# Kernel optimization log

Measured on AMD Instinct MI355X. Metric: run time of the kernel, lower is better.

Reference implementation:

```python
import jax, jax.numpy as jnp
import numpy as np

N = 100000      # nodes
E = 1_600_000   # edges (avg degree 16)
IN, HID, OUT = 128, 128, 64


def _prep(edge_index, n):
    """Add self-loops and compute symmetric GCN normalization per edge."""
    loops = jnp.arange(n, dtype=edge_index.dtype)
    src = jnp.concatenate([edge_index[0], loops])  # [E+N]
    dst = jnp.concatenate([edge_index[1], loops])  # [E+N]
    deg = jax.ops.segment_sum(jnp.ones(src.shape, jnp.float32), dst, num_segments=n)
    dinv = jnp.where(deg > 0, jax.lax.rsqrt(deg), 0.0)
    norm = dinv[src] * dinv[dst]                   # [E+N]
    return src, dst, norm


def gcn_conv(x, src, dst, norm, W, b, n):
    # PyG GCNConv: transform first, then normalized gather/scatter-add aggregate
    h = x @ W                                      # [N, C_out]
    msg = h[src] * norm[:, None]                   # [E+N, C_out] irregular gather
    return jax.ops.segment_sum(msg, dst, num_segments=n) + b


def setup_inputs() -> dict:
    key = jax.random.key(0)
    k1, k2, k3, k4 = jax.random.split(key, 4)
    x = jax.random.normal(k1, (N, IN), dtype=jnp.float32)
    edge_index = jax.random.randint(k2, (2, E), 0, N, dtype=jnp.int32)
    W1 = jax.random.normal(k3, (IN, HID), dtype=jnp.float32) * (1.0 / np.sqrt(IN))
    b1 = jnp.zeros((HID,), jnp.float32)
    W2 = jax.random.normal(k4, (HID, OUT), dtype=jnp.float32) * (1.0 / np.sqrt(HID))
    b2 = jnp.zeros((OUT,), jnp.float32)
    return {"x": x, "W1": W1, "b1": b1, "W2": W2, "b2": b2, "edge_index": edge_index}


def reference(x, W1, b1, W2, b2, edge_index):
    n = x.shape[0]
    src, dst, norm = _prep(edge_index, n)
    h = gcn_conv(x, src, dst, norm, W1, b1, n)
    h = jax.nn.softmax(h, axis=1)
    return gcn_conv(h, src, dst, norm, W2, b2, n)
```

## Files before the change

kernel.cpp:

```cpp
#include <hip/hip_runtime.h>
#include <hip/hip_fp16.h>
#include <cstdint>
#include <cstddef>


#define BSHIFT 8
#define NBPAD 512
#define NWG 256
#define CAP 6144

typedef _Float16 half8 __attribute__((ext_vector_type(8)));
typedef float f32x4 __attribute__((ext_vector_type(4)));

__device__ __forceinline__ void h8_to_f(const uint4& u, float* f) {
  const __half2* hp = (const __half2*)&u;
#pragma unroll
  for (int i = 0; i < 4; ++i) {
    float2 t = __half22float2(hp[i]);
    f[2 * i] = t.x;
    f[2 * i + 1] = t.y;
  }
}

__device__ __forceinline__ void fma8(float* acc, float w, const float* v) {
#pragma unroll
  for (int i = 0; i < 8; ++i) acc[i] = fmaf(w, v[i], acc[i]);
}

__device__ __forceinline__ int block_scan256(int v, int* wsums) {
  const int lane = threadIdx.x & 63;
  const int wid = threadIdx.x >> 6;
  int x = v;
#pragma unroll
  for (int d = 1; d < 64; d <<= 1) {
    int y = __shfl_up(x, d);
    if (lane >= d) x += y;
  }
  if (lane == 63) wsums[wid] = x;
  __syncthreads();
  int off = 0;
#pragma unroll
  for (int j = 0; j < 4; ++j)
    if (j < wid) off += wsums[j];
  return off + x;
}

__global__ __launch_bounds__(256) void wg_count(const int* __restrict__ dst,
                                                int* __restrict__ counts,
                                                int E, int nb, int slice) {
  __shared__ int lh[NBPAD];
  const int w = blockIdx.x;
  for (int i = threadIdx.x; i < nb; i += 256) lh[i] = 0;
  __syncthreads();
  const int e0 = w * slice;
  const int e1 = min(e0 + slice, E);
  for (int e = e0 + threadIdx.x; e < e1; e += 256)
    atomicAdd(&lh[dst[e] >> BSHIFT], 1);
  __syncthreads();
  for (int i = threadIdx.x; i < nb; i += 256) counts[(size_t)w * NBPAD + i] = lh[i];
}

__global__ __launch_bounds__(1024) void scan_buckets(const int* __restrict__ counts,
                                                     int* __restrict__ bstart,
                                                     int* __restrict__ row_start,
                                                     int nb, int n, int E) {
  __shared__ int wsum[16];
  const int tid = threadIdx.x;
  const int lane = tid & 63;
  const int wid = tid >> 6;
  int v = 0;
  if (tid < nb) {
#pragma unroll 4
    for (int i = 0; i < NWG; ++i) v += counts[(size_t)i * NBPAD + tid];
  }
  int x = v;
#pragma unroll
  for (int d = 1; d < 64; d <<= 1) {
    int y = __shfl_up(x, d);
    if (lane >= d) x += y;
  }
  if (lane == 63) wsum[wid] = x;
  __syncthreads();
  if (wid == 0) {
    int w = (lane < 16) ? wsum[lane] : 0;
#pragma unroll
    for (int d = 1; d < 16; d <<= 1) {
      int y = __shfl_up(w, d);
      if (lane >= d) w += y;
    }
    if (lane < 16) wsum[lane] = w;
  }
  __syncthreads();
  int boff = (wid > 0) ? wsum[wid - 1] : 0;
  int incl = boff + x;
  if (tid < nb) {
    bstart[tid] = incl - v;
    if (tid == nb - 1) bstart[nb] = incl;
  }
  if (tid == 0) row_start[n] = E;
}

__global__ __launch_bounds__(256) void cell_scan(const int* __restrict__ counts,
                                                 const int* __restrict__ bstart,
                                                 int* __restrict__ cur, int nb) {
  __shared__ int wsums[4];
  const int b = blockIdx.x;
  const int tid = threadIdx.x;
  int v = counts[(size_t)tid * NBPAD + b];
  int incl = block_scan256(v, wsums);
  cur[(size_t)tid * NBPAD + b] = bstart[b] + incl - v;
}

__global__ __launch_bounds__(256) void wg_scatter(const int* __restrict__ src,
                                                  const int* __restrict__ dst,
                                                  const int* __restrict__ cur,
                                                  unsigned* __restrict__ staging,
                                                  int E, int nb, int slice) {
  __shared__ int lc[NBPAD];
  const int w = blockIdx.x;
  for (int i = threadIdx.x; i < nb; i += 256) lc[i] = cur[(size_t)w * NBPAD + i];
  __syncthreads();
  const int e0 = w * slice;
  const int e1 = min(e0 + slice, E);
  for (int e = e0 + threadIdx.x; e < e1; e += 256) {
    int d = dst[e];
    int p = atomicAdd(&lc[d >> BSHIFT], 1);
    staging[p] = ((unsigned)(d & 255) << 24) | (unsigned)src[e];
  }
}

__global__ __launch_bounds__(256) void bucket_hist(const unsigned* __restrict__ staging,
                                                   const int* __restrict__ bstart,
                                                   int* __restrict__ row_start,
                                                   float* __restrict__ dinv, int n) {
  __shared__ int lcnt[256];
  __shared__ int wsums[4];
  const int b = blockIdx.x;
  const int tid = threadIdx.x;
  const int n0 = b << BSHIFT;
  const int s0 = bstart[b];
  const int cnt = bstart[b + 1] - s0;

  lcnt[tid] = 0;
  __syncthreads();
  for (int i = tid; i < cnt; i += 256)
    atomicAdd(&lcnt[staging[s0 + i] >> 24], 1);
  __syncthreads();

  const int v = lcnt[tid];
  const int incl = block_scan256(v, wsums);
  const int node = n0 + tid;
  if (node < n) {
    row_start[node] = s0 + incl - v;
    dinv[node] = rsqrtf((float)v + 1.0f);
  }
}

__global__ __launch_bounds__(256) void bucket_pack(const unsigned* __restrict__ staging,
                                                   const int* __restrict__ bstart,
                                                   const int* __restrict__ row_start,
                                                   const float* __restrict__ dinv,
                                                   int2* __restrict__ pack, int n) {
  __shared__ int lcur[256];
  __shared__ int lbuf[CAP];
  const int b = blockIdx.x;
  const int tid = threadIdx.x;
  const int n0 = b << BSHIFT;
  const int s0 = bstart[b];
  const int cnt = bstart[b + 1] - s0;

  const int node = n0 + tid;
  lcur[tid] = (node < n) ? (row_start[node] - s0) : 0;
  __syncthreads();

  for (int i = tid; i < cnt; i += 256) {
    unsigned p = staging[s0 + i];
    int pos = atomicAdd(&lcur[p >> 24], 1);
    int s = (int)(p & 0xFFFFFFu);
    if (pos < CAP) lbuf[pos] = s;
    else pack[s0 + pos] = make_int2(s, __float_as_int(dinv[s]));
  }
  __syncthreads();
  const int lim = cnt < CAP ? cnt : CAP;
  for (int i = tid; i < lim; i += 256) {
    int s = lbuf[i];
    pack[s0 + i] = make_int2(s, __float_as_int(dinv[s]));
  }
}

template <int M>
__global__ __launch_bounds__(256) void pack_w(const float* __restrict__ W,
                                              _Float16* __restrict__ Wp) {
  int e = blockIdx.x * 256 + threadIdx.x;
  if (e < 128 * M) {
    int k = e / M, c = e % M;
    int t = k >> 5, g = (k >> 3) & 3, j = k & 7;
    Wp[(((size_t)t * M + c) * 4 + g) * 8 + j] = (_Float16)W[e];
  }
}

template <int M, bool HIN>
__global__ __launch_bounds__(256) void gemm_mfma(const void* __restrict__ Xp,
                                                 const _Float16* __restrict__ Wp,
                                                 _Float16* __restrict__ H, int N) {
  constexpr int CT = M / 16;
  const int wave = threadIdx.x >> 6;
  const int lane = threadIdx.x & 63;
  const int row0 = (blockIdx.x * 4 + wave) * 16;
  if (row0 >= N) return;
  const int r = lane & 15;
  const int g = lane >> 4;
  int row = row0 + r;
  if (row >= N) row = N - 1;

  f32x4 acc[CT];
#pragma unroll
  for (int c = 0; c < CT; ++c) acc[c] = (f32x4){0.f, 0.f, 0.f, 0.f};

#pragma unroll
  for (int t = 0; t < 4; ++t) {
    half8 a;
    if constexpr (HIN) {
      a = *(const half8*)((const _Float16*)Xp + (size_t)row * 128 + t * 32 + g * 8);
    } else {
      const float* xp = (const float*)Xp + (size_t)row * 128 + t * 32 + g * 8;
      float4 x0 = *(const float4*)xp;
      float4 x1 = *(const float4*)(xp + 4);
      a[0] = (_Float16)x0.x; a[1] = (_Float16)x0.y;
      a[2] = (_Float16)x0.z; a[3] = (_Float16)x0.w;
      a[4] = (_Float16)x1.x; a[5] = (_Float16)x1.y;
      a[6] = (_Float16)x1.z; a[7] = (_Float16)x1.w;
    }
#pragma unroll
    for (int c = 0; c < CT; ++c) {
      half8 b = *(const half8*)(Wp + (((size_t)t * M + c * 16 + r) * 4 + g) * 8);
      acc[c] = __builtin_amdgcn_mfma_f32_16x16x32_f16(a, b, acc[c], 0, 0, 0);
    }
  }

#pragma unroll
  for (int c = 0; c < CT; ++c) {
#pragma unroll
    for (int i = 0; i < 4; ++i) {
      int rr = row0 + 4 * g + i;
      if (rr < N) H[(size_t)rr * M + c * 16 + r] = (_Float16)acc[c][i];
    }
  }
}

__device__ __forceinline__ void pack_batch(const int2* __restrict__ pack,
                                           int e, int e1, int2* p) {
#pragma unroll
  for (int j = 0; j < 4; ++j) {
    int idx = e + j;
    bool ok = idx < e1;
    p[j] = pack[ok ? idx : (e1 - 1)];
    if (!ok) p[j].y = 0;
  }
}

template <int F, bool SM, bool OUTHALF>
__global__ __launch_bounds__(256) void aggregate(const __half* __restrict__ h,
                                                 const int* __restrict__ row_start,
                                                 const int2* __restrict__ pack,
                                                 const float* __restrict__ dinv,
                                                 const float* __restrict__ bias,
                                                 void* __restrict__ out, int n) {
  constexpr int LPG = F / 8;
  constexpr int GPB = 256 / LPG;
  const int node = blockIdx.x * GPB + (int)(threadIdx.x / LPG);
  const int lane = threadIdx.x % LPG;
  if (node >= n) return;

  const uint4* hv = (const uint4*)h;
  const float di = dinv[node];

  float acc[8];
  {
    uint4 su = hv[(size_t)node * LPG + lane];
    float sf[8];
    h8_to_f(su, sf);
#pragma unroll
    for (int i = 0; i < 8; ++i) acc[i] = di * sf[i];
  }

  const int e0 = row_start[node];
  const int e1 = row_start[node + 1];
  if (e0 < e1) {
    int2 p[4];
    pack_batch(pack, e0, e1, p);
    int e = e0;
    for (;;) {
      uint4 r[4];
#pragma unroll
      for (int j = 0; j < 4; ++j) r[j] = hv[(size_t)p[j].x * LPG + lane];
      const int en = e + 4;
      const bool more = en < e1;
      int2 pn[4];
      if (more) pack_batch(pack, en, e1, pn);
#pragma unroll
      for (int j = 0; j < 4; ++j) {
        float v[8];
        h8_to_f(r[j], v);
        fma8(acc, __int_as_float(p[j].y), v);
      }
      if (!more) break;
#pragma unroll
      for (int j = 0; j < 4; ++j) p[j] = pn[j];
      e = en;
    }
  }

  {
    const float4* bv = (const float4*)bias;
    float4 b0 = bv[lane * 2], b1 = bv[lane * 2 + 1];
    acc[0] = fmaf(di, acc[0], b0.x);
    acc[1] = fmaf(di, acc[1], b0.y);
    acc[2] = fmaf(di, acc[2], b0.z);
    acc[3] = fmaf(di, acc[3], b0.w);
    acc[4] = fmaf(di, acc[4], b1.x);
    acc[5] = fmaf(di, acc[5], b1.y);
    acc[6] = fmaf(di, acc[6], b1.z);
    acc[7] = fmaf(di, acc[7], b1.w);
  }

  if constexpr (SM) {
    float m = acc[0];
#pragma unroll
    for (int i = 1; i < 8; ++i) m = fmaxf(m, acc[i]);
#pragma unroll
    for (int off = LPG / 2; off >= 1; off >>= 1) m = fmaxf(m, __shfl_xor(m, off));
    float ex[8], ssum = 0.f;
#pragma unroll
    for (int i = 0; i < 8; ++i) {
      ex[i] = __expf(acc[i] - m);
      ssum += ex[i];
    }
#pragma unroll
    for (int off = LPG / 2; off >= 1; off >>= 1) ssum += __shfl_xor(ssum, off);
    float r = 1.0f / ssum;
#pragma unroll
    for (int i = 0; i < 8; ++i) acc[i] = ex[i] * r;
  }

  if constexpr (OUTHALF) {
    union { __half2 h2[4]; uint4 u; } cv;
#pragma unroll
    for (int i = 0; i < 4; ++i)
      cv.h2[i] = __floats2half2_rn(acc[2 * i], acc[2 * i + 1]);
    ((uint4*)out)[(size_t)node * LPG + lane] = cv.u;
  } else {
    float4* ov = (float4*)out;
    ov[(size_t)node * (F / 4) + lane * 2] =
        make_float4(acc[0], acc[1], acc[2], acc[3]);
    ov[(size_t)node * (F / 4) + lane * 2 + 1] =
        make_float4(acc[4], acc[5], acc[6], acc[7]);
  }
}

extern "C" void kernel_launch(void* const* d_in, const int* in_sizes, int n_in,
                              void* d_out, int out_size, void* d_ws, size_t ws_size,
                              hipStream_t stream) {
  const float* x  = (const float*)d_in[0];
  const float* W1 = (const float*)d_in[1];
  const float* b1 = (const float*)d_in[2];
  const float* W2 = (const float*)d_in[3];
  const float* b2 = (const float*)d_in[4];
  const int*   ei = (const int*)d_in[5];

  const int N = in_sizes[0] / 128;
  const int E = in_sizes[5] / 2;
  const int NB = (N + 255) >> BSHIFT;
  const int SLICE = (E + NWG - 1) / NWG;
  const int* srcp = ei;
  const int* dstp = ei + E;

  auto align256 = [](size_t v) { return (v + 255) & ~(size_t)255; };
  char* ws = (char*)d_ws;
  size_t o_dinv   = 0;
  size_t o_rs     = align256(o_dinv + (size_t)N * 4);
  size_t o_cnts   = align256(o_rs + (size_t)(N + 1) * 4);
  size_t o_cur    = align256(o_cnts + (size_t)NWG * NBPAD * 4);
  size_t o_bstart = align256(o_cur + (size_t)NWG * NBPAD * 4);
  size_t o_wp1    = align256(o_bstart + (size_t)(NBPAD + 1) * 4);
  size_t o_wp2    = align256(o_wp1 + (size_t)128 * 128 * 2);
  size_t o_stg    = align256(o_wp2 + (size_t)128 * 64 * 2);
  size_t o_pack   = align256(o_stg + (size_t)E * 4);
  size_t o_h1     = align256(o_pack + (size_t)E * 8);
  size_t o_s      = align256(o_h1 + (size_t)N * 128 * 2);

  float*    dinv     = (float*)(ws + o_dinv);
  int*      rowstart = (int*)(ws + o_rs);
  int*      counts   = (int*)(ws + o_cnts);
  int*      cur      = (int*)(ws + o_cur);
  int*      bstart   = (int*)(ws + o_bstart);
  _Float16* wp1      = (_Float16*)(ws + o_wp1);
  _Float16* wp2      = (_Float16*)(ws + o_wp2);
  unsigned* staging  = (unsigned*)(ws + o_stg);
  int2*     pack     = (int2*)(ws + o_pack);
  _Float16* h1       = (_Float16*)(ws + o_h1);
  _Float16* sbuf     = (_Float16*)(ws + o_s);

  wg_count<<<NWG, 256, 0, stream>>>(dstp, counts, E, NB, SLICE);
  scan_buckets<<<1, 1024, 0, stream>>>(counts, bstart, rowstart, NB, N, E);
  cell_scan<<<NB, 256, 0, stream>>>(counts, bstart, cur, NB);
  wg_scatter<<<NWG, 256, 0, stream>>>(srcp, dstp, cur, staging, E, NB, SLICE);
  bucket_hist<<<NB, 256, 0, stream>>>(staging, bstart, rowstart, dinv, N);
  bucket_pack<<<NB, 256, 0, stream>>>(staging, bstart, rowstart, dinv, pack, N);

  pack_w<128><<<(128 * 128 + 255) / 256, 256, 0, stream>>>(W1, wp1);
  pack_w<64><<<(128 * 64 + 255) / 256, 256, 0, stream>>>(W2, wp2);

  gemm_mfma<128, false><<<(N + 63) / 64, 256, 0, stream>>>(x, wp1, h1, N);
  aggregate<128, true, true><<<(N + 15) / 16, 256, 0, stream>>>(
      (const __half*)h1, rowstart, pack, dinv, b1, sbuf, N);
  gemm_mfma<64, true><<<(N + 63) / 64, 256, 0, stream>>>(sbuf, wp2, h1, N);
  aggregate<64, false, false><<<(N + 31) / 32, 256, 0, stream>>>(
      (const __half*)h1, rowstart, pack, dinv, b2, d_out, N);
}
```

Baseline: 202.7 us.

## Reorder bucket scan to avoid serial column sum and double-buffer aggregate gathers

The single-block bucket scan no longer sums 256 count rows per thread serially. Per-bucket column scans now run first across many blocks and emit bucket totals, a small single-block scan produces bucket starts, and the scatter kernel adds the start when loading its cursors. The aggregate kernel's neighbor loop is now software-pipelined two batches deep, so edge-pack loads and feature gathers for the next batch are issued before the current batch is accumulated. This raises register pressure in aggregate and adds one small workspace buffer.

```diff
diff --git a/kernel.cpp b/kernel.cpp
--- a/kernel.cpp
+++ b/kernel.cpp
@@ -60,19 +60,27 @@
   for (int i = threadIdx.x; i < nb; i += 256) counts[(size_t)w * NBPAD + i] = lh[i];
 }
 
-__global__ __launch_bounds__(1024) void scan_buckets(const int* __restrict__ counts,
-                                                     int* __restrict__ bstart,
-                                                     int* __restrict__ row_start,
-                                                     int nb, int n, int E) {
+__global__ __launch_bounds__(256) void cell_scan(const int* __restrict__ counts,
+                                                 int* __restrict__ cur,
+                                                 int* __restrict__ btotal, int nb) {
+  __shared__ int wsums[4];
+  const int b = blockIdx.x;
+  const int tid = threadIdx.x;
+  int v = counts[(size_t)tid * NBPAD + b];
+  int incl = block_scan256(v, wsums);
+  cur[(size_t)tid * NBPAD + b] = incl - v;
+  if (tid == 255) btotal[b] = incl;
+}
+
+__global__ __launch_bounds__(1024) void bscan(const int* __restrict__ btotal,
+                                              int* __restrict__ bstart,
+                                              int* __restrict__ row_start,
+                                              int nb, int n, int E) {
   __shared__ int wsum[16];
   const int tid = threadIdx.x;
   const int lane = tid & 63;
   const int wid = tid >> 6;
-  int v = 0;
-  if (tid < nb) {
-#pragma unroll 4
-    for (int i = 0; i < NWG; ++i) v += counts[(size_t)i * NBPAD + tid];
-  }
+  int v = (tid < nb) ? btotal[tid] : 0;
   int x = v;
 #pragma unroll
   for (int d = 1; d < 64; d <<= 1) {
@@ -100,25 +108,16 @@
   if (tid == 0) row_start[n] = E;
 }
 
-__global__ __launch_bounds__(256) void cell_scan(const int* __restrict__ counts,
-                                                 const int* __restrict__ bstart,
-                                                 int* __restrict__ cur, int nb) {
-  __shared__ int wsums[4];
-  const int b = blockIdx.x;
-  const int tid = threadIdx.x;
-  int v = counts[(size_t)tid * NBPAD + b];
-  int incl = block_scan256(v, wsums);
-  cur[(size_t)tid * NBPAD + b] = bstart[b] + incl - v;
-}
-
 __global__ __launch_bounds__(256) void wg_scatter(const int* __restrict__ src,
                                                   const int* __restrict__ dst,
                                                   const int* __restrict__ cur,
+                                                  const int* __restrict__ bstart,
                                                   unsigned* __restrict__ staging,
                                                   int E, int nb, int slice) {
   __shared__ int lc[NBPAD];
   const int w = blockIdx.x;
-  for (int i = threadIdx.x; i < nb; i += 256) lc[i] = cur[(size_t)w * NBPAD + i];
+  for (int i = threadIdx.x; i < nb; i += 256)
+    lc[i] = cur[(size_t)w * NBPAD + i] + bstart[i];
   __syncthreads();
   const int e0 = w * slice;
   const int e1 = min(e0 + slice, E);
@@ -286,28 +285,36 @@
 
   const int e0 = row_start[node];
   const int e1 = row_start[node + 1];
-  if (e0 < e1) {
-    int2 p[4];
-    pack_batch(pack, e0, e1, p);
-    int e = e0;
-    for (;;) {
-      uint4 r[4];
-#pragma unroll
-      for (int j = 0; j < 4; ++j) r[j] = hv[(size_t)p[j].x * LPG + lane];
-      const int en = e + 4;
-      const bool more = en < e1;
-      int2 pn[4];
-      if (more) pack_batch(pack, en, e1, pn);
+  const int nbat = (e1 - e0 + 3) >> 2;
+
+  if (nbat > 0) {
+    int2 p0[4], p1[4];
+    uint4 r0[4];
+    pack_batch(pack, e0, e1, p0);
+#pragma unroll
+    for (int j = 0; j < 4; ++j) r0[j] = hv[(size_t)p0[j].x * LPG + lane];
+    if (nbat > 1) pack_batch(pack, e0 + 4, e1, p1);
+
+    for (int k = 0; k < nbat; ++k) {
+      uint4 r1[4];
+      if (k + 1 < nbat) {
+#pragma unroll
+        for (int j = 0; j < 4; ++j) r1[j] = hv[(size_t)p1[j].x * LPG + lane];
+      }
+      int2 p2[4];
+      if (k + 2 < nbat) pack_batch(pack, e0 + 4 * (k + 2), e1, p2);
 #pragma unroll
       for (int j = 0; j < 4; ++j) {
         float v[8];
-        h8_to_f(r[j], v);
-        fma8(acc, __int_as_float(p[j].y), v);
+        h8_to_f(r0[j], v);
+        fma8(acc, __int_as_float(p0[j].y), v);
       }
-      if (!more) break;
-#pragma unroll
-      for (int j = 0; j < 4; ++j) p[j] = pn[j];
-      e = en;
+#pragma unroll
+      for (int j = 0; j < 4; ++j) {
+        p0[j] = p1[j];
+        p1[j] = p2[j];
+        r0[j] = r1[j];
+      }
     }
   }
 
@@ -381,7 +388,8 @@
   size_t o_rs     = align256(o_dinv + (size_t)N * 4);
   size_t o_cnts   = align256(o_rs + (size_t)(N + 1) * 4);
   size_t o_cur    = align256(o_cnts + (size_t)NWG * NBPAD * 4);
-  size_t o_bstart = align256(o_cur + (size_t)NWG * NBPAD * 4);
+  size_t o_btot   = align256(o_cur + (size_t)NWG * NBPAD * 4);
+  size_t o_bstart = align256(o_btot + (size_t)NBPAD * 4);
   size_t o_wp1    = align256(o_bstart + (size_t)(NBPAD + 1) * 4);
   size_t o_wp2    = align256(o_wp1 + (size_t)128 * 128 * 2);
   size_t o_stg    = align256(o_wp2 + (size_t)128 * 64 * 2);
@@ -393,6 +401,7 @@
   int*      rowstart = (int*)(ws + o_rs);
   int*      counts   = (int*)(ws + o_cnts);
   int*      cur      = (int*)(ws + o_cur);
+  int*      btotal   = (int*)(ws + o_btot);
   int*      bstart   = (int*)(ws + o_bstart);
   _Float16* wp1      = (_Float16*)(ws + o_wp1);
   _Float16* wp2      = (_Float16*)(ws + o_wp2);
@@ -402,9 +411,9 @@
   _Float16* sbuf     = (_Float16*)(ws + o_s);
 
   wg_count<<<NWG, 256, 0, stream>>>(dstp, counts, E, NB, SLICE);
-  scan_buckets<<<1, 1024, 0, stream>>>(counts, bstart, rowstart, NB, N, E);
-  cell_scan<<<NB, 256, 0, stream>>>(counts, bstart, cur, NB);
-  wg_scatter<<<NWG, 256, 0, stream>>>(srcp, dstp, cur, staging, E, NB, SLICE);
+  cell_scan<<<NB, 256, 0, stream>>>(counts, cur, btotal, NB);
+  bscan<<<1, 1024, 0, stream>>>(btotal, bstart, rowstart, NB, N, E);
+  wg_scatter<<<NWG, 256, 0, stream>>>(srcp, dstp, cur, bstart, staging, E, NB, SLICE);
   bucket_hist<<<NB, 256, 0, stream>>>(staging, bstart, rowstart, dinv, N);
   bucket_pack<<<NB, 256, 0, stream>>>(staging, bstart, rowstart, dinv, pack, N);
 
```

After: 192.4 us. -5.1%, faster.
